# Performance work log

Hardware: AMD Instinct MI355X
Metric: run time of the kernel (lower is better)

Reference implementation:

```python
import jax, jax.numpy as jnp
import numpy as np

N_NODES = 100000
N_EDGES = 1000000
NODE_DIM = 128
EDGE_DIM = 64
IN_DIM = 2 * NODE_DIM + EDGE_DIM  # 320


def _linear_init(key, fan_in, fan_out):
    # mimic torch nn.Linear default: U(-1/sqrt(fan_in), 1/sqrt(fan_in))
    kw, kb = jax.random.split(key)
    bound = 1.0 / np.sqrt(fan_in)
    W = jax.random.uniform(kw, (fan_in, fan_out), jnp.float32, -bound, bound)
    b = jax.random.uniform(kb, (fan_out,), jnp.float32, -bound, bound)
    return W, b


def setup_inputs() -> dict:
    key = jax.random.key(0)
    ks = jax.random.split(key, 8)
    x = jax.random.normal(ks[0], (N_NODES, NODE_DIM), jnp.float32)
    edge_index = jax.random.randint(ks[1], (2, N_EDGES), 0, N_NODES, jnp.int64 if jax.config.read('jax_enable_x64') else jnp.int32)
    edge_features = jax.random.normal(ks[2], (N_EDGES, EDGE_DIM), jnp.float32)
    W1, b1 = _linear_init(ks[3], IN_DIM, 256)
    W2, b2 = _linear_init(ks[4], 256, 128)
    W3, b3 = _linear_init(ks[5], 128, 64)
    W4, b4 = _linear_init(ks[6], 64, 1)
    return {
        'x': x, 'edge_index': edge_index, 'edge_features': edge_features,
        'num_nodes': N_NODES,
        'W1': W1, 'b1': b1, 'W2': W2, 'b2': b2,
        'W3': W3, 'b3': b3, 'W4': W4, 'b4': b4,
    }


def reference(x, edge_index, edge_features, num_nodes, W1, b1, W2, b2, W3, b3, W4, b4):
    v = edge_index[0]
    u = edge_index[1]
    # gather endpoint embeddings and concat with edge features: [E, 2*node_dim+edge_dim]
    pair = jnp.concatenate([x[v], x[u], edge_features], axis=-1)
    h = jax.nn.relu(pair @ W1 + b1)
    h = jax.nn.relu(h @ W2 + b2)
    h = jax.nn.relu(h @ W3 + b3)
    pred = h @ W4 + b4  # [E, 1]
    return pred
```

## Files before the change

### kernel.cpp

```cpp
#include <hip/hip_runtime.h>
#include <hip/hip_bf16.h>

typedef __bf16 bf16;
typedef __attribute__((ext_vector_type(8))) __bf16 bf16x8;
typedef __attribute__((ext_vector_type(4))) __bf16 bf16x4;
typedef __attribute__((ext_vector_type(4))) float f32x4;

#define E_TOTAL   1000000
#define NODE_DIM  128
#define EDGE_DIM  64

#define SA_STRIDE  328
#define SH1_STRIDE 264
#define SH2_STRIDE 136
#define SH3_STRIDE 72

#define SMEM_BYTES 51200
#define SH2_OFF    33792

#define WS_XBF_BYTES 25600000
#define WB_W2F  163840
#define WB_W3F  (163840 + 65536)
#define WB_CANO (163840 + 65536 + 16384)
#define WB_FLAG (163840 + 65536 + 16384 + 2052)
#define WB_END  (163840 + 65536 + 16384 + 2052 + 16)
#define WS_NEED (WS_XBF_BYTES + WB_END)

__device__ inline int plausible16(const unsigned short* h) {
    int c = 0;
    for (int i = 0; i < 64; ++i) {
        int e = (h[i] >> 7) & 0xFF;
        if (e >= 90 && e <= 151) ++c;
    }
    return c;
}

__global__ void sniff(const void* x, const void* ei, const void* ef,
                      const void* W1, int* flags) {
    if (threadIdx.x == 0 && blockIdx.x == 0) {
        flags[0] = (plausible16((const unsigned short*)x)  < 52) ? 1 : 0;
        flags[1] = (plausible16((const unsigned short*)ef) < 52) ? 1 : 0;
        flags[2] = (plausible16((const unsigned short*)W1) < 52) ? 1 : 0;
        const int* w = (const int*)ei;
        int oz = 0, lo_ok = 1;
        for (int i = 1; i < 32; i += 2) if (w[i] == 0) ++oz;
        for (int i = 0; i < 32; i += 2) if ((unsigned)w[i] >= 100000u) lo_ok = 0;
        flags[3] = (oz == 16 && lo_ok) ? 1 : 0;
    }
}

__device__ inline float loadF(const void* p, int isf, int i) {
    return isf ? ((const float*)p)[i] : (float)((const bf16*)p)[i];
}

__global__ void canonicalize(const void* W1, const void* W2, const void* W3,
                             const void* b1, const void* b2, const void* b3,
                             const void* W4, const void* b4,
                             bf16* W1f, bf16* W2f, bf16* W3f,
                             float* cano, const int* flags) {
    int isf = flags[2];
    int o = blockIdx.x * 256 + threadIdx.x;
    if (o < 81920) {
        int jj = o & 7, lane = (o >> 3) & 63, t2 = o >> 9;
        int ks = t2 % 10, jt = t2 / 10;
        int k = ks * 32 + (lane >> 4) * 8 + jj;
        int n = jt * 16 + (lane & 15);
        W1f[o] = (bf16)loadF(W1, isf, k * 256 + n);
    } else if (o < 114688) {
        int o2 = o - 81920;
        int jj = o2 & 7, lane = (o2 >> 3) & 63, t2 = o2 >> 9;
        int ks = t2 & 7, jt = t2 >> 3;
        int k = ks * 32 + (lane >> 4) * 8 + jj;
        int n = jt * 16 + (lane & 15);
        W2f[o2] = (bf16)loadF(W2, isf, k * 128 + n);
    } else if (o < 122880) {
        int o3 = o - 114688;
        int jj = o3 & 7, lane = (o3 >> 3) & 63, t2 = o3 >> 9;
        int ks = t2 & 3, jt = t2 >> 2;
        int k = ks * 32 + (lane >> 4) * 8 + jj;
        int n = jt * 16 + (lane & 15);
        W3f[o3] = (bf16)loadF(W3, isf, k * 64 + n);
    } else if (o < 123393) {
        int j = o - 122880;
        float v;
        if (j < 256)       v = loadF(b1, isf, j);
        else if (j < 384)  v = loadF(b2, isf, j - 256);
        else if (j < 448)  v = loadF(b3, isf, j - 384);
        else if (j == 448) v = loadF(b4, isf, 0);
        else               v = loadF(W4, isf, j - 449);
        cano[j] = v;
    }
}

__global__ void convert_x(const void* x, bf16* xbf, const int* flags) {
    int i = (blockIdx.x * 256 + threadIdx.x) * 4;
    if (flags[0]) {
        const float* f = (const float*)x + i;
        bf16 v0 = (bf16)f[0], v1 = (bf16)f[1], v2 = (bf16)f[2], v3 = (bf16)f[3];
        xbf[i] = v0; xbf[i + 1] = v1; xbf[i + 2] = v2; xbf[i + 3] = v3;
    } else {
        *(unsigned long long*)(xbf + i) = *(const unsigned long long*)((const bf16*)x + i);
    }
}

__global__ __launch_bounds__(256, 3) void fused_mlp(
    const void* __restrict__ xs, const int* __restrict__ ei, const void* __restrict__ ef,
    const bf16* __restrict__ W1f, const bf16* __restrict__ W2f,
    const bf16* __restrict__ W3f,
    const float* __restrict__ cano, const int* __restrict__ flags,
    int xmode_host, float* __restrict__ out)
{
    __shared__ __align__(16) char smem[SMEM_BYTES];
    bf16* sA  = (bf16*)smem;
    bf16* sH1 = (bf16*)smem;
    bf16* sH2 = (bf16*)(smem + SH2_OFF);
    bf16* sH3 = (bf16*)smem;

    const int tid  = threadIdx.x;
    const int wave = tid >> 6;
    const int lane = tid & 63;
    const int quad = lane >> 4;
    const int l16  = lane & 15;
    const int e0   = blockIdx.x * 64;

    const int isfe = flags[1];
    const int is64 = flags[3];
    const int xm   = (xmode_host < 0) ? flags[0] : xmode_host;

    {
        const int xrow0 = tid >> 5;
        const int xseg  = tid & 31;
        const int which = xseg >> 4;
        const int xk    = (xseg & 15) << 3;
        if (xm == 0) {
            const bf16* xsb = (const bf16*)xs;
            bf16x8 xb[8];
#pragma unroll
            for (int i = 0; i < 8; ++i) {
                int row = i * 8 + xrow0;
                size_t pos = which ? (size_t)(E_TOTAL + e0 + row) : (size_t)(e0 + row);
                int node = is64 ? ei[2 * pos] : ei[pos];
                xb[i] = *(const bf16x8*)(xsb + (size_t)node * NODE_DIM + xk);
            }
#pragma unroll
            for (int i = 0; i < 8; ++i)
                *(bf16x8*)&sA[(i * 8 + xrow0) * SA_STRIDE + xseg * 8] = xb[i];
        } else {
            const float* xsf = (const float*)xs;
            float xf[8][8];
#pragma unroll
            for (int i = 0; i < 8; ++i) {
                int row = i * 8 + xrow0;
                size_t pos = which ? (size_t)(E_TOTAL + e0 + row) : (size_t)(e0 + row);
                int node = is64 ? ei[2 * pos] : ei[pos];
                const float* f = xsf + (size_t)node * NODE_DIM + xk;
#pragma unroll
                for (int j = 0; j < 8; ++j) xf[i][j] = f[j];
            }
#pragma unroll
            for (int i = 0; i < 8; ++i) {
                bf16x8 v;
#pragma unroll
                for (int j = 0; j < 8; ++j) v[j] = (bf16)xf[i][j];
                *(bf16x8*)&sA[(i * 8 + xrow0) * SA_STRIDE + xseg * 8] = v;
            }
        }
        int seg = tid & 7, r0 = tid >> 3, r1 = r0 + 32;
        int kst = 256 + seg * 8;
        if (isfe) {
            const float* f0 = (const float*)ef + (size_t)(e0 + r0) * EDGE_DIM + seg * 8;
            const float* f1 = (const float*)ef + (size_t)(e0 + r1) * EDGE_DIM + seg * 8;
            float a0[8], a1[8];
#pragma unroll
            for (int j = 0; j < 8; ++j) { a0[j] = f0[j]; a1[j] = f1[j]; }
            bf16x8 v0, v1;
#pragma unroll
            for (int j = 0; j < 8; ++j) { v0[j] = (bf16)a0[j]; v1[j] = (bf16)a1[j]; }
            *(bf16x8*)&sA[r0 * SA_STRIDE + kst] = v0;
            *(bf16x8*)&sA[r1 * SA_STRIDE + kst] = v1;
        } else {
            const bf16* eb = (const bf16*)ef;
            bf16x8 v0 = *(const bf16x8*)(eb + (size_t)(e0 + r0) * EDGE_DIM + seg * 8);
            bf16x8 v1 = *(const bf16x8*)(eb + (size_t)(e0 + r1) * EDGE_DIM + seg * 8);
            *(bf16x8*)&sA[r0 * SA_STRIDE + kst] = v0;
            *(bf16x8*)&sA[r1 * SA_STRIDE + kst] = v1;
        }
    }
    __syncthreads();

    f32x4 acc1[4][4];
#pragma unroll
    for (int p = 0; p < 4; ++p)
#pragma unroll
        for (int q = 0; q < 4; ++q)
            acc1[p][q] = (f32x4){0.f, 0.f, 0.f, 0.f};

    const bf16* w1base = W1f + (size_t)wave * (40 * 512) + lane * 8;
#pragma unroll
    for (int ks = 0; ks < 10; ++ks) {
        bf16x8 w[4], e[4];
#pragma unroll
        for (int p = 0; p < 4; ++p)
            w[p] = *(const bf16x8*)(w1base + (p * 10 + ks) * 512);
#pragma unroll
        for (int q = 0; q < 4; ++q)
            e[q] = *(const bf16x8*)&sA[(16 * q + l16) * SA_STRIDE + ks * 32 + quad * 8];
#pragma unroll
        for (int p = 0; p < 4; ++p)
#pragma unroll
            for (int q = 0; q < 4; ++q)
                acc1[p][q] = __builtin_amdgcn_mfma_f32_16x16x32_bf16(
                    w[p], e[q], acc1[p][q], 0, 0, 0);
    }
    __syncthreads();
    {
#pragma unroll
        for (int p = 0; p < 4; ++p) {
            f32x4 bias = *(const f32x4*)&cano[64 * wave + 16 * p + 4 * quad];
#pragma unroll
            for (int q = 0; q < 4; ++q) {
                bf16x4 pv;
#pragma unroll
                for (int r = 0; r < 4; ++r)
                    pv[r] = (bf16)fmaxf(acc1[p][q][r] + bias[r], 0.f);
                *(bf16x4*)&sH1[(16 * q + l16) * SH1_STRIDE + 64 * wave + 16 * p + 4 * quad] = pv;
            }
        }
    }
    __syncthreads();

    f32x4 acc2[2][4];
#pragma unroll
    for (int p = 0; p < 2; ++p)
#pragma unroll
        for (int q = 0; q < 4; ++q)
            acc2[p][q] = (f32x4){0.f, 0.f, 0.f, 0.f};
    const bf16* w2base = W2f + (size_t)wave * (16 * 512) + lane * 8;
#pragma unroll
    for (int ks = 0; ks < 8; ++ks) {
        bf16x8 w[2], e[4];
#pragma unroll
        for (int p = 0; p < 2; ++p)
            w[p] = *(const bf16x8*)(w2base + (p * 8 + ks) * 512);
#pragma unroll
        for (int q = 0; q < 4; ++q)
            e[q] = *(const bf16x8*)&sH1[(16 * q + l16) * SH1_STRIDE + ks * 32 + quad * 8];
#pragma unroll
        for (int p = 0; p < 2; ++p)
#pragma unroll
            for (int q = 0; q < 4; ++q)
                acc2[p][q] = __builtin_amdgcn_mfma_f32_16x16x32_bf16(
                    w[p], e[q], acc2[p][q], 0, 0, 0);
    }
    {
#pragma unroll
        for (int p = 0; p < 2; ++p) {
            f32x4 bias = *(const f32x4*)&cano[256 + 32 * wave + 16 * p + 4 * quad];
#pragma unroll
            for (int q = 0; q < 4; ++q) {
                bf16x4 pv;
#pragma unroll
                for (int r = 0; r < 4; ++r)
                    pv[r] = (bf16)fmaxf(acc2[p][q][r] + bias[r], 0.f);
                *(bf16x4*)&sH2[(16 * q + l16) * SH2_STRIDE + 32 * wave + 16 * p + 4 * quad] = pv;
            }
        }
    }
    __syncthreads();

    f32x4 acc3[4];
#pragma unroll
    for (int q = 0; q < 4; ++q) acc3[q] = (f32x4){0.f, 0.f, 0.f, 0.f};
    const bf16* w3base = W3f + (size_t)wave * (4 * 512) + lane * 8;
#pragma unroll
    for (int ks = 0; ks < 4; ++ks) {
        bf16x8 w = *(const bf16x8*)(w3base + ks * 512);
#pragma unroll
        for (int q = 0; q < 4; ++q) {
            bf16x8 e = *(const bf16x8*)&sH2[(16 * q + l16) * SH2_STRIDE + ks * 32 + quad * 8];
            acc3[q] = __builtin_amdgcn_mfma_f32_16x16x32_bf16(w, e, acc3[q], 0, 0, 0);
        }
    }
    {
        f32x4 bias = *(const f32x4*)&cano[384 + 16 * wave + 4 * quad];
#pragma unroll
        for (int q = 0; q < 4; ++q) {
            bf16x4 pv;
#pragma unroll
            for (int r = 0; r < 4; ++r)
                pv[r] = (bf16)fmaxf(acc3[q][r] + bias[r], 0.f);
            *(bf16x4*)&sH3[(16 * q + l16) * SH3_STRIDE + 16 * wave + 4 * quad] = pv;
        }
    }
    __syncthreads();

    {
        int edge = tid >> 2;
        int part = tid & 3;
        int k0 = part * 16;
        const bf16* h = &sH3[edge * SH3_STRIDE + k0];
        bf16x8 h0 = *(const bf16x8*)h;
        bf16x8 h1 = *(const bf16x8*)(h + 8);
        float s = 0.f;
#pragma unroll
        for (int k = 0; k < 8; ++k) s += (float)h0[k] * cano[449 + k0 + k];
#pragma unroll
        for (int k = 0; k < 8; ++k) s += (float)h1[k] * cano[449 + k0 + 8 + k];
        s += __shfl_xor(s, 1);
        s += __shfl_xor(s, 2);
        if (part == 0) out[e0 + edge] = s + cano[448];
    }
}

extern "C" void kernel_launch(void* const* d_in, const int* in_sizes, int n_in,
                              void* d_out, int out_size, void* d_ws, size_t ws_size,
                              hipStream_t stream) {
    const void* x  = d_in[0];
    const int*  ei = (const int*)d_in[1];
    const void* ef = d_in[2];
    const void* W1 = d_in[4];
    const void* b1 = d_in[5];
    const void* W2 = d_in[6];
    const void* b2 = d_in[7];
    const void* W3 = d_in[8];
    const void* b3 = d_in[9];
    const void* W4 = d_in[10];
    const void* b4 = d_in[11];
    float* out = (float*)d_out;

    char* ws = (char*)d_ws;
    const bool big = ws_size >= (size_t)WS_NEED;
    bf16* xbf   = (bf16*)ws;
    char* wbase = big ? (ws + WS_XBF_BYTES) : ws;
    bf16*  W1f   = (bf16*)wbase;
    bf16*  W2f   = (bf16*)(wbase + WB_W2F);
    bf16*  W3f   = (bf16*)(wbase + WB_W3F);
    float* cano  = (float*)(wbase + WB_CANO);
    int*   flags = (int*)(wbase + WB_FLAG);

    sniff<<<1, 64, 0, stream>>>(x, ei, ef, W1, flags);
    canonicalize<<<483, 256, 0, stream>>>(W1, W2, W3, b1, b2, b3, W4, b4,
                                          W1f, W2f, W3f, cano, flags);
    if (big) convert_x<<<12500, 256, 0, stream>>>(x, xbf, flags);
    fused_mlp<<<E_TOTAL / 64, 256, 0, stream>>>(
        big ? (const void*)xbf : x, ei, ef, W1f, W2f, W3f,
        cano, flags, big ? 0 : -1, out);
}
```

Baseline: 632.7 us.

## Add persistent fused MLP kernel with register prefetch of next tile's gathers

Adds a persistent kernel launched with a fixed grid that loops over 64-edge tiles. Each iteration prefetches the next tile's edge indices during layer 1 and its node and edge feature gathers during layer 2, so gather latency overlaps MFMA work. The W4 entries in the canonical constant buffer are shifted to a 16-byte-aligned offset, with the old kernel updated to match. The prefetch buffers add register pressure that could lower occupancy, and the fixed grid may leave compute units unevenly loaded.

```diff
diff --git a/kernel.cpp b/kernel.cpp
--- a/kernel.cpp
+++ b/kernel.cpp
@@ -7,6 +7,8 @@
 typedef __attribute__((ext_vector_type(4))) float f32x4;
 
 #define E_TOTAL   1000000
+#define N_TILES   15625
+#define PGRID     768
 #define NODE_DIM  128
 #define EDGE_DIM  64
 
@@ -22,8 +24,8 @@
 #define WB_W2F  163840
 #define WB_W3F  (163840 + 65536)
 #define WB_CANO (163840 + 65536 + 16384)
-#define WB_FLAG (163840 + 65536 + 16384 + 2052)
-#define WB_END  (163840 + 65536 + 16384 + 2052 + 16)
+#define WB_FLAG (163840 + 65536 + 16384 + 2064)
+#define WB_END  (163840 + 65536 + 16384 + 2064 + 16)
 #define WS_NEED (WS_XBF_BYTES + WB_END)
 
 __device__ inline int plausible16(const unsigned short* h) {
@@ -80,14 +82,15 @@
         int k = ks * 32 + (lane >> 4) * 8 + jj;
         int n = jt * 16 + (lane & 15);
         W3f[o3] = (bf16)loadF(W3, isf, k * 64 + n);
-    } else if (o < 123393) {
+    } else if (o < 123396) {
         int j = o - 122880;
         float v;
         if (j < 256)       v = loadF(b1, isf, j);
         else if (j < 384)  v = loadF(b2, isf, j - 256);
         else if (j < 448)  v = loadF(b3, isf, j - 384);
         else if (j == 448) v = loadF(b4, isf, 0);
-        else               v = loadF(W4, isf, j - 449);
+        else if (j < 452)  v = 0.f;
+        else               v = loadF(W4, isf, j - 452);
         cano[j] = v;
     }
 }
@@ -100,6 +103,246 @@
         xbf[i] = v0; xbf[i + 1] = v1; xbf[i + 2] = v2; xbf[i + 3] = v3;
     } else {
         *(unsigned long long*)(xbf + i) = *(const unsigned long long*)((const bf16*)x + i);
+    }
+}
+
+__global__ __launch_bounds__(256, 3) void fused_mlp_persist(
+    const bf16* __restrict__ xs, const int* __restrict__ ei, const void* __restrict__ ef,
+    const bf16* __restrict__ W1f, const bf16* __restrict__ W2f,
+    const bf16* __restrict__ W3f,
+    const float* __restrict__ cano, const int* __restrict__ flags,
+    float* __restrict__ out)
+{
+    __shared__ __align__(16) char smem[SMEM_BYTES];
+    bf16* sA  = (bf16*)smem;
+    bf16* sH1 = (bf16*)smem;
+    bf16* sH2 = (bf16*)(smem + SH2_OFF);
+    bf16* sH3 = (bf16*)smem;
+
+    const int tid  = threadIdx.x;
+    const int wave = tid >> 6;
+    const int lane = tid & 63;
+    const int quad = lane >> 4;
+    const int l16  = lane & 15;
+
+    const int isfe = flags[1];
+    const int is64 = flags[3];
+
+    const int xrow0 = tid >> 5;
+    const int xseg  = tid & 31;
+    const int which = xseg >> 4;
+    const int xk    = (xseg & 15) << 3;
+    const int eseg  = tid & 7;
+    const int er0   = tid >> 3;
+    const int er1   = er0 + 32;
+
+    int t = blockIdx.x;
+
+    int    nidx[8];
+    bf16x8 xb[8];
+    float  efa[8], efb[8];
+    bf16x8 efv0, efv1;
+
+    {
+        const int e0 = t * 64;
+#pragma unroll
+        for (int i = 0; i < 8; ++i) {
+            size_t pos = which ? (size_t)(E_TOTAL + e0 + i * 8 + xrow0)
+                               : (size_t)(e0 + i * 8 + xrow0);
+            nidx[i] = is64 ? ei[2 * pos] : ei[pos];
+        }
+#pragma unroll
+        for (int i = 0; i < 8; ++i)
+            xb[i] = *(const bf16x8*)(xs + (size_t)nidx[i] * NODE_DIM + xk);
+        if (isfe) {
+            const float* f0 = (const float*)ef + (size_t)(e0 + er0) * EDGE_DIM + eseg * 8;
+            const float* f1 = (const float*)ef + (size_t)(e0 + er1) * EDGE_DIM + eseg * 8;
+#pragma unroll
+            for (int j = 0; j < 8; ++j) { efa[j] = f0[j]; efb[j] = f1[j]; }
+        } else {
+            const bf16* eb = (const bf16*)ef;
+            efv0 = *(const bf16x8*)(eb + (size_t)(t * 64 + er0) * EDGE_DIM + eseg * 8);
+            efv1 = *(const bf16x8*)(eb + (size_t)(t * 64 + er1) * EDGE_DIM + eseg * 8);
+        }
+    }
+
+    while (true) {
+        const int e0 = t * 64;
+
+#pragma unroll
+        for (int i = 0; i < 8; ++i)
+            *(bf16x8*)&sA[(i * 8 + xrow0) * SA_STRIDE + xseg * 8] = xb[i];
+        {
+            const int kst = 256 + eseg * 8;
+            if (isfe) {
+                bf16x8 v0, v1;
+#pragma unroll
+                for (int j = 0; j < 8; ++j) { v0[j] = (bf16)efa[j]; v1[j] = (bf16)efb[j]; }
+                *(bf16x8*)&sA[er0 * SA_STRIDE + kst] = v0;
+                *(bf16x8*)&sA[er1 * SA_STRIDE + kst] = v1;
+            } else {
+                *(bf16x8*)&sA[er0 * SA_STRIDE + kst] = efv0;
+                *(bf16x8*)&sA[er1 * SA_STRIDE + kst] = efv1;
+            }
+        }
+        __syncthreads();
+
+        const int  tn   = t + PGRID;
+        const bool more = tn < N_TILES;
+
+        if (more) {
+            const int en = tn * 64;
+#pragma unroll
+            for (int i = 0; i < 8; ++i) {
+                size_t pos = which ? (size_t)(E_TOTAL + en + i * 8 + xrow0)
+                                   : (size_t)(en + i * 8 + xrow0);
+                nidx[i] = is64 ? ei[2 * pos] : ei[pos];
+            }
+        }
+
+        f32x4 acc1[4][4];
+#pragma unroll
+        for (int p = 0; p < 4; ++p)
+#pragma unroll
+            for (int q = 0; q < 4; ++q)
+                acc1[p][q] = (f32x4){0.f, 0.f, 0.f, 0.f};
+
+        const bf16* w1base = W1f + (size_t)wave * (40 * 512) + lane * 8;
+#pragma unroll
+        for (int ks = 0; ks < 10; ++ks) {
+            bf16x8 w[4], e[4];
+#pragma unroll
+            for (int p = 0; p < 4; ++p)
+                w[p] = *(const bf16x8*)(w1base + (p * 10 + ks) * 512);
+#pragma unroll
+            for (int q = 0; q < 4; ++q)
+                e[q] = *(const bf16x8*)&sA[(16 * q + l16) * SA_STRIDE + ks * 32 + quad * 8];
+#pragma unroll
+            for (int p = 0; p < 4; ++p)
+#pragma unroll
+                for (int q = 0; q < 4; ++q)
+                    acc1[p][q] = __builtin_amdgcn_mfma_f32_16x16x32_bf16(
+                        w[p], e[q], acc1[p][q], 0, 0, 0);
+        }
+        __syncthreads();
+        {
+#pragma unroll
+            for (int p = 0; p < 4; ++p) {
+                f32x4 bias = *(const f32x4*)&cano[64 * wave + 16 * p + 4 * quad];
+#pragma unroll
+                for (int q = 0; q < 4; ++q) {
+                    bf16x4 pv;
+#pragma unroll
+                    for (int r = 0; r < 4; ++r)
+                        pv[r] = (bf16)fmaxf(acc1[p][q][r] + bias[r], 0.f);
+                    *(bf16x4*)&sH1[(16 * q + l16) * SH1_STRIDE + 64 * wave + 16 * p + 4 * quad] = pv;
+                }
+            }
+        }
+        __syncthreads();
+
+        if (more) {
+#pragma unroll
+            for (int i = 0; i < 8; ++i)
+                xb[i] = *(const bf16x8*)(xs + (size_t)nidx[i] * NODE_DIM + xk);
+            const int en = tn * 64;
+            if (isfe) {
+                const float* f0 = (const float*)ef + (size_t)(en + er0) * EDGE_DIM + eseg * 8;
+                const float* f1 = (const float*)ef + (size_t)(en + er1) * EDGE_DIM + eseg * 8;
+#pragma unroll
+                for (int j = 0; j < 8; ++j) { efa[j] = f0[j]; efb[j] = f1[j]; }
+            } else {
+                const bf16* eb = (const bf16*)ef;
+                efv0 = *(const bf16x8*)(eb + (size_t)(en + er0) * EDGE_DIM + eseg * 8);
+                efv1 = *(const bf16x8*)(eb + (size_t)(en + er1) * EDGE_DIM + eseg * 8);
+            }
+        }
+
+        f32x4 acc2[2][4];
+#pragma unroll
+        for (int p = 0; p < 2; ++p)
+#pragma unroll
+            for (int q = 0; q < 4; ++q)
+                acc2[p][q] = (f32x4){0.f, 0.f, 0.f, 0.f};
+        const bf16* w2base = W2f + (size_t)wave * (16 * 512) + lane * 8;
+#pragma unroll
+        for (int ks = 0; ks < 8; ++ks) {
+            bf16x8 w[2], e[4];
+#pragma unroll
+            for (int p = 0; p < 2; ++p)
+                w[p] = *(const bf16x8*)(w2base + (p * 8 + ks) * 512);
+#pragma unroll
+            for (int q = 0; q < 4; ++q)
+                e[q] = *(const bf16x8*)&sH1[(16 * q + l16) * SH1_STRIDE + ks * 32 + quad * 8];
+#pragma unroll
+            for (int p = 0; p < 2; ++p)
+#pragma unroll
+                for (int q = 0; q < 4; ++q)
+                    acc2[p][q] = __builtin_amdgcn_mfma_f32_16x16x32_bf16(
+                        w[p], e[q], acc2[p][q], 0, 0, 0);
+        }
+        {
+#pragma unroll
+            for (int p = 0; p < 2; ++p) {
+                f32x4 bias = *(const f32x4*)&cano[256 + 32 * wave + 16 * p + 4 * quad];
+#pragma unroll
+                for (int q = 0; q < 4; ++q) {
+                    bf16x4 pv;
+#pragma unroll
+                    for (int r = 0; r < 4; ++r)
+                        pv[r] = (bf16)fmaxf(acc2[p][q][r] + bias[r], 0.f);
+                    *(bf16x4*)&sH2[(16 * q + l16) * SH2_STRIDE + 32 * wave + 16 * p + 4 * quad] = pv;
+                }
+            }
+        }
+        __syncthreads();
+
+        f32x4 acc3[4];
+#pragma unroll
+        for (int q = 0; q < 4; ++q) acc3[q] = (f32x4){0.f, 0.f, 0.f, 0.f};
+        const bf16* w3base = W3f + (size_t)wave * (4 * 512) + lane * 8;
+#pragma unroll
+        for (int ks = 0; ks < 4; ++ks) {
+            bf16x8 w = *(const bf16x8*)(w3base + ks * 512);
+#pragma unroll
+            for (int q = 0; q < 4; ++q) {
+                bf16x8 e = *(const bf16x8*)&sH2[(16 * q + l16) * SH2_STRIDE + ks * 32 + quad * 8];
+                acc3[q] = __builtin_amdgcn_mfma_f32_16x16x32_bf16(w, e, acc3[q], 0, 0, 0);
+            }
+        }
+        {
+            f32x4 bias = *(const f32x4*)&cano[384 + 16 * wave + 4 * quad];
+#pragma unroll
+            for (int q = 0; q < 4; ++q) {
+                bf16x4 pv;
+#pragma unroll
+                for (int r = 0; r < 4; ++r)
+                    pv[r] = (bf16)fmaxf(acc3[q][r] + bias[r], 0.f);
+                *(bf16x4*)&sH3[(16 * q + l16) * SH3_STRIDE + 16 * wave + 4 * quad] = pv;
+            }
+        }
+        __syncthreads();
+
+        {
+            int edge = tid >> 2;
+            int part = tid & 3;
+            int k0 = part * 16;
+            const bf16* h = &sH3[edge * SH3_STRIDE + k0];
+            bf16x8 h0 = *(const bf16x8*)h;
+            bf16x8 h1 = *(const bf16x8*)(h + 8);
+            float s = 0.f;
+#pragma unroll
+            for (int k = 0; k < 8; ++k) s += (float)h0[k] * cano[452 + k0 + k];
+#pragma unroll
+            for (int k = 0; k < 8; ++k) s += (float)h1[k] * cano[452 + k0 + 8 + k];
+            s += __shfl_xor(s, 1);
+            s += __shfl_xor(s, 2);
+            if (part == 0) out[e0 + edge] = s + cano[448];
+        }
+
+        if (!more) break;
+        __syncthreads();
+        t = tn;
     }
 }
 
@@ -303,9 +546,9 @@
         bf16x8 h1 = *(const bf16x8*)(h + 8);
         float s = 0.f;
 #pragma unroll
-        for (int k = 0; k < 8; ++k) s += (float)h0[k] * cano[449 + k0 + k];
-#pragma unroll
-        for (int k = 0; k < 8; ++k) s += (float)h1[k] * cano[449 + k0 + 8 + k];
+        for (int k = 0; k < 8; ++k) s += (float)h0[k] * cano[452 + k0 + k];
+#pragma unroll
+        for (int k = 0; k < 8; ++k) s += (float)h1[k] * cano[452 + k0 + 8 + k];
         s += __shfl_xor(s, 1);
         s += __shfl_xor(s, 2);
         if (part == 0) out[e0 + edge] = s + cano[448];
@@ -341,8 +584,12 @@
     sniff<<<1, 64, 0, stream>>>(x, ei, ef, W1, flags);
     canonicalize<<<483, 256, 0, stream>>>(W1, W2, W3, b1, b2, b3, W4, b4,
                                           W1f, W2f, W3f, cano, flags);
-    if (big) convert_x<<<12500, 256, 0, stream>>>(x, xbf, flags);
-    fused_mlp<<<E_TOTAL / 64, 256, 0, stream>>>(
-        big ? (const void*)xbf : x, ei, ef, W1f, W2f, W3f,
-        cano, flags, big ? 0 : -1, out);
-}
+    if (big) {
+        convert_x<<<12500, 256, 0, stream>>>(x, xbf, flags);
+        fused_mlp_persist<<<PGRID, 256, 0, stream>>>(
+            xbf, ei, ef, W1f, W2f, W3f, cano, flags, out);
+    } else {
+        fused_mlp<<<E_TOTAL / 64, 256, 0, stream>>>(
+            x, ei, ef, W1f, W2f, W3f, cano, flags, -1, out);
+    }
+}
```

Measured after the change: 1.578 ms. 2.49x slower.
